# Kernel optimization log

Measured on AMD Instinct MI355X. Metric: run time of the kernel, lower is better.

## Reference

```python
import jax, jax.numpy as jnp
import numpy as np

B, T, D, E = 4096, 64, 256, 4
H = D * E  # hidden width per token position


def setup_inputs() -> dict:
    key = jax.random.key(0)
    kx, k1, kb1, k2, kb2 = jax.random.split(key, 5)
    # torch.nn.Linear default init ~ U(-1/sqrt(fan_in), 1/sqrt(fan_in)); scaled normals are fine for a numeric reference
    x = jax.random.normal(kx, (B, T, D), dtype=jnp.float32)
    W1 = jax.random.normal(k1, (T, D, H), dtype=jnp.float32) / np.sqrt(D)
    b1 = jax.random.normal(kb1, (T, H), dtype=jnp.float32) / np.sqrt(D)
    W2 = jax.random.normal(k2, (T, H, D), dtype=jnp.float32) / np.sqrt(H)
    b2 = jax.random.normal(kb2, (T, D), dtype=jnp.float32) / np.sqrt(H)
    return {"x": x, "W1": W1, "b1": b1, "W2": W2, "b2": b2}


def reference(x, W1, b1, W2, b2):
    # Per-position MLP with distinct weights: grouped GEMM over the T axis.
    h = jnp.einsum('btd,tdh->bth', x, W1) + b1          # [B, T, H]
    h = jax.nn.gelu(h, approximate=False)                # torch GELU default = exact erf form
    out = jnp.einsum('bth,thd->btd', h, W2) + b2         # [B, T, D]
    return out
```

## Files before the change

### kernel.cpp

```cpp
#include <hip/hip_runtime.h>


typedef __bf16 bf16x8 __attribute__((ext_vector_type(8)));
typedef float  floatx4 __attribute__((ext_vector_type(4)));

__device__ __forceinline__ unsigned short f2bf(float f) {
  unsigned u = __builtin_bit_cast(unsigned, f);
  u += 0x7fffu + ((u >> 16) & 1u);
  return (unsigned short)(u >> 16);
}

__device__ __forceinline__ float gelu_exact(float v) {
  return 0.5f * v * (1.0f + erff(v * 0.70710678118654752f));
}

__device__ __forceinline__ void gll16(const void* g, void* l) {
  __builtin_amdgcn_global_load_lds(
      (const __attribute__((address_space(1))) unsigned*)g,
      (__attribute__((address_space(3))) unsigned*)(unsigned)(unsigned long long)l,
      16, 0, 0);
}

__device__ __forceinline__ void barrier_fenced() {
  asm volatile("" ::: "memory");
  __builtin_amdgcn_s_barrier();
  asm volatile("" ::: "memory");
}


__global__ __launch_bounds__(256) void prep_w1(const float* __restrict__ w1,
                                               unsigned short* __restrict__ img) {
  const int idx  = blockIdx.x * 256 + threadIdx.x;
  const int slot = idx & 511;
  const int im   = idx >> 9;
  const int jl = slot >> 2, m = slot & 3;
  const int kk = im & 7, c = (im >> 3) & 7, t = im >> 6;
  const int q  = m ^ ((jl >> 1) & 3);
  const float* src = w1 + (size_t)t * 262144 +
                     (size_t)(kk * 32 + q * 8) * 1024 + c * 128 + jl;
  union { uint4 v; unsigned short s[8]; } o;
#pragma unroll
  for (int i = 0; i < 8; ++i) o.s[i] = f2bf(src[(size_t)i * 1024]);
  *(uint4*)(img + (size_t)idx * 8) = o.v;
}

__global__ __launch_bounds__(256) void prep_w2(const float* __restrict__ w2,
                                               unsigned short* __restrict__ img) {
  const int idx  = blockIdx.x * 256 + threadIdx.x;
  const int slot = idx & 1023;
  const int im   = idx >> 10;
  const int d = slot >> 2, m = slot & 3;
  const int kk2 = im & 3, c = (im >> 2) & 7, t = im >> 5;
  const int q   = m ^ ((d >> 1) & 3);
  const float* src = w2 + (size_t)t * 262144 +
                     (size_t)(c * 128 + kk2 * 32 + q * 8) * 256 + d;
  union { uint4 v; unsigned short s[8]; } o;
#pragma unroll
  for (int i = 0; i < 8; ++i) o.s[i] = f2bf(src[(size_t)i * 256]);
  *(uint4*)(img + (size_t)idx * 8) = o.v;
}

__global__ __launch_bounds__(256)
__attribute__((amdgpu_waves_per_eu(2, 2)))
void mlp_fast(
    const float* __restrict__ x, const unsigned short* __restrict__ w1i,
    const float* __restrict__ b1, const unsigned short* __restrict__ w2i,
    const float* __restrict__ b2, float* __restrict__ out) {

  __shared__ __attribute__((aligned(16))) unsigned char lds[69632];
  unsigned char* const w1b0 = lds;
  unsigned char* const w1b1 = lds + 8192;
  unsigned char* const w2b0 = lds + 16384;
  unsigned char* const w2b1 = lds + 32768;
  unsigned char* const hlds = lds + 49152;
  float* const b1lds = (float*)(lds + 65536);

  const int tid  = threadIdx.x;
  const int lane = tid & 63;
  const int w    = tid >> 6;
  const int wm   = w >> 1;
  const int wn   = w & 1;
  const int l15  = lane & 15;
  const int l4   = lane >> 4;

  const int bid  = blockIdx.x;
  const int t    = (bid & 7) + 8 * (bid >> 9);
  const int b0   = ((bid >> 3) & 63) << 6;

  const unsigned char* w1t = (const unsigned char*)(w1i + (size_t)t * 262144);
  const unsigned char* w2t = (const unsigned char*)(w2i + (size_t)t * 262144);
  const int lo16 = lane * 16;

#pragma unroll
  for (int i = 0; i < 4; ++i)
    b1lds[tid + 256 * i] = b1[t * 1024 + tid + 256 * i];

  bf16x8 xfrag[2][8];
#pragma unroll
  for (int mt = 0; mt < 2; ++mt) {
    const int b = b0 + wm * 32 + mt * 16 + l15;
    const float* xb = x + ((size_t)b * 64 + t) * 256 + l4 * 8;
#pragma unroll
    for (int kk = 0; kk < 8; ++kk) {
      floatx4 lo = *(const floatx4*)(xb + kk * 32);
      floatx4 hi = *(const floatx4*)(xb + kk * 32 + 4);
      union { bf16x8 v; unsigned short s[8]; } px;
      px.s[0] = f2bf(lo[0]); px.s[1] = f2bf(lo[1]);
      px.s[2] = f2bf(lo[2]); px.s[3] = f2bf(lo[3]);
      px.s[4] = f2bf(hi[0]); px.s[5] = f2bf(hi[1]);
      px.s[6] = f2bf(hi[2]); px.s[7] = f2bf(hi[3]);
      xfrag[mt][kk] = px.v;
    }
  }

  floatx4 oacc[4][4];
#pragma unroll
  for (int mt = 0; mt < 4; ++mt) {
    const floatx4 bv = *(const floatx4*)(b2 + t * 256 + w * 64 + mt * 16 + l4 * 4);
#pragma unroll
    for (int nt = 0; nt < 4; ++nt) oacc[mt][nt] = bv;
  }

  const int swf    = (l4 ^ ((lane >> 1) & 3)) << 4;
  const int w1base = ((wn * 64 + l15) << 6) + swf;
  const int w2base = ((w * 64 + l15) << 6) + swf;

  auto stageW1 = [&](int cc, int kk, unsigned char* buf) {
    const unsigned char* s = w1t + (((cc << 3) + kk) << 13) + (w << 11) + lo16;
    unsigned char* d = buf + (w << 11);
    gll16(s, d);
    gll16(s + 1024, d + 1024);
  };
  auto stageW2 = [&](int cc, int k2, unsigned char* buf) {
    const unsigned char* s = w2t + (((cc << 2) + k2) << 14) + (w << 12) + lo16;
    unsigned char* d = buf + (w << 12);
    gll16(s, d);               gll16(s + 1024, d + 1024);
    gll16(s + 2048, d + 2048); gll16(s + 3072, d + 3072);
  };

  stageW1(0, 0, w1b0);
  __syncthreads();

#pragma unroll 1
  for (int c = 0; c < 8; ++c) {
    floatx4 hacc[2][4];
#pragma unroll
    for (int nt = 0; nt < 4; ++nt) {
      const float bv = b1lds[c * 128 + wn * 64 + nt * 16 + l15];
      const floatx4 bb = {bv, bv, bv, bv};
      hacc[0][nt] = bb; hacc[1][nt] = bb;
    }

#pragma unroll
    for (int k = 0; k < 8; ++k) {
      if (k < 7) {
        stageW1(c, k + 1, ((k + 1) & 1) ? w1b1 : w1b0);
        asm volatile("s_waitcnt vmcnt(2)" ::: "memory");
      } else {
        stageW2(c, 0, w2b0);
        asm volatile("s_waitcnt vmcnt(4)" ::: "memory");
      }
      barrier_fenced();

      const unsigned char* rb = (k & 1) ? w1b1 : w1b0;
      bf16x8 bfrag[4];
#pragma unroll
      for (int nt = 0; nt < 4; ++nt)
        bfrag[nt] = *(const bf16x8*)(rb + w1base + nt * 1024);
      __builtin_amdgcn_s_setprio(1);
#pragma unroll
      for (int mt = 0; mt < 2; ++mt)
#pragma unroll
        for (int nt = 0; nt < 4; ++nt)
          hacc[mt][nt] = __builtin_amdgcn_mfma_f32_16x16x32_bf16(
              xfrag[mt][k], bfrag[nt], hacc[mt][nt], 0, 0, 0);
      __builtin_amdgcn_s_setprio(0);
      barrier_fenced();
    }

#pragma unroll
    for (int mt = 0; mt < 2; ++mt)
#pragma unroll
      for (int nt = 0; nt < 4; ++nt) {
        const int jl = wn * 64 + nt * 16 + l15;
        const int q  = jl >> 3;
        const int jo = (jl & 7) * 2;
#pragma unroll
        for (int r = 0; r < 4; ++r) {
          const float g = gelu_exact(hacc[mt][nt][r]);
          const int b = wm * 32 + mt * 16 + l4 * 4 + r;
          *(unsigned short*)(hlds + b * 256 + ((q ^ (b & 7)) * 16) + jo) = f2bf(g);
        }
      }

#pragma unroll
    for (int k2 = 0; k2 < 4; ++k2) {
      if (k2 < 3) {
        stageW2(c, k2 + 1, ((k2 + 1) & 1) ? w2b1 : w2b0);
        if (k2 == 0)
          asm volatile("s_waitcnt vmcnt(4) lgkmcnt(0)" ::: "memory");
        else
          asm volatile("s_waitcnt vmcnt(4)" ::: "memory");
      } else {
        if (c < 7) {
          stageW1(c + 1, 0, w1b0);
          asm volatile("s_waitcnt vmcnt(2)" ::: "memory");
        } else {
          asm volatile("s_waitcnt vmcnt(0)" ::: "memory");
        }
      }
      barrier_fenced();

      const unsigned char* rb = (k2 & 1) ? w2b1 : w2b0;
      bf16x8 afrag[4];
#pragma unroll
      for (int mt = 0; mt < 4; ++mt)
        afrag[mt] = *(const bf16x8*)(rb + w2base + mt * 1024);
      bf16x8 hfrag[4];
#pragma unroll
      for (int nt = 0; nt < 4; ++nt)
        hfrag[nt] = *(const bf16x8*)(hlds + (nt * 16 + l15) * 256 +
                                     (((k2 * 4 + l4) ^ (lane & 7)) * 16));
      __builtin_amdgcn_s_setprio(1);
#pragma unroll
      for (int mt = 0; mt < 4; ++mt)
#pragma unroll
        for (int nt = 0; nt < 4; ++nt)
          oacc[mt][nt] = __builtin_amdgcn_mfma_f32_16x16x32_bf16(
              afrag[mt], hfrag[nt], oacc[mt][nt], 0, 0, 0);
      __builtin_amdgcn_s_setprio(0);
      barrier_fenced();
    }
  }

#pragma unroll
  for (int mt = 0; mt < 4; ++mt) {
    const int d = w * 64 + mt * 16 + l4 * 4;
#pragma unroll
    for (int nt = 0; nt < 4; ++nt) {
      const int b = b0 + nt * 16 + l15;
      *(floatx4*)(out + ((size_t)b * 64 + t) * 256 + d) = oacc[mt][nt];
    }
  }
}

__global__ __launch_bounds__(256, 2) void mlp_kernel(
    const float* __restrict__ x, const float* __restrict__ w1,
    const float* __restrict__ b1, const float* __restrict__ w2,
    const float* __restrict__ b2, float* __restrict__ out) {

  __shared__ __attribute__((aligned(16))) unsigned char lds[40960];
  unsigned char* const w1img = lds;
  unsigned char* const w2img = lds + 8192;
  unsigned char* const hlds  = lds + 24576;

  const int tid  = threadIdx.x;
  const int lane = tid & 63;
  const int w    = tid >> 6;
  const int wm   = w >> 1;
  const int wn   = w & 1;
  const int l15  = lane & 15;
  const int l4   = lane >> 4;

  const int bid  = blockIdx.x;
  const int t    = (bid & 7) + 8 * (bid >> 9);
  const int b0   = ((bid >> 3) & 63) << 6;

  const float* w1t = w1 + (size_t)t * 262144;
  const float* w2t = w2 + (size_t)t * 262144;

  const int jl_s   = tid & 127;
  const int half_s = tid >> 7;
  const int P_s    = half_s ^ ((jl_s >> 2) & 1);
  const int sw2s   = (tid >> 1) & 3;

  bf16x8 xfrag[2][8];
#pragma unroll
  for (int mt = 0; mt < 2; ++mt) {
    const int b = b0 + wm * 32 + mt * 16 + l15;
    const float* xb = x + ((size_t)b * 64 + t) * 256 + l4 * 8;
#pragma unroll
    for (int kk = 0; kk < 8; ++kk) {
      floatx4 lo = *(const floatx4*)(xb + kk * 32);
      floatx4 hi = *(const floatx4*)(xb + kk * 32 + 4);
      union { bf16x8 v; unsigned short s[8]; } px;
      px.s[0] = f2bf(lo[0]); px.s[1] = f2bf(lo[1]);
      px.s[2] = f2bf(lo[2]); px.s[3] = f2bf(lo[3]);
      px.s[4] = f2bf(hi[0]); px.s[5] = f2bf(hi[1]);
      px.s[6] = f2bf(hi[2]); px.s[7] = f2bf(hi[3]);
      xfrag[mt][kk] = px.v;
    }
  }

  floatx4 oacc[4][4];
#pragma unroll
  for (int mt = 0; mt < 4; ++mt) {
    const floatx4 bv = *(const floatx4*)(b2 + t * 256 + w * 64 + mt * 16 + l4 * 4);
#pragma unroll
    for (int nt = 0; nt < 4; ++nt) oacc[mt][nt] = bv;
  }

  const int swf    = (l4 ^ ((lane >> 1) & 3)) << 4;
  const int w1base = ((wn * 64 + l15) << 6) + swf;
  const int w2base = ((w * 64 + l15) << 6) + swf;

#pragma unroll 1
  for (int c = 0; c < 8; ++c) {
    floatx4 hacc[2][4];
#pragma unroll
    for (int nt = 0; nt < 4; ++nt) {
      const float bv = b1[t * 1024 + c * 128 + wn * 64 + nt * 16 + l15];
      const floatx4 bb = {bv, bv, bv, bv};
      hacc[0][nt] = bb; hacc[1][nt] = bb;
    }

#pragma unroll
    for (int kk = 0; kk < 8; ++kk) {
      float f[16];
      const float* src = w1t + (size_t)(kk * 32 + half_s * 16) * 1024 + c * 128 + jl_s;
#pragma unroll
      for (int u = 0; u < 16; ++u) f[u] = src[(size_t)u * 1024];

      __syncthreads();
      union { uint4 v; unsigned short s[8]; } pk[2];
#pragma unroll
      for (int u = 0; u < 16; ++u) pk[u >> 3].s[u & 7] = f2bf(f[u]);
#pragma unroll
      for (int p = 0; p < 2; ++p) {
        const int m = 2 * P_s + p;
        const int s = (p ^ (jl_s >> 1)) & 1;
        *(uint4*)(w1img + jl_s * 64 + m * 16) = pk[s].v;
      }
      __syncthreads();

      bf16x8 bfrag[4];
#pragma unroll
      for (int nt = 0; nt < 4; ++nt)
        bfrag[nt] = *(const bf16x8*)(w1img + w1base + nt * 1024);
#pragma unroll
      for (int mt = 0; mt < 2; ++mt)
#pragma unroll
        for (int nt = 0; nt < 4; ++nt)
          hacc[mt][nt] = __builtin_amdgcn_mfma_f32_16x16x32_bf16(
              xfrag[mt][kk], bfrag[nt], hacc[mt][nt], 0, 0, 0);
    }

#pragma unroll
    for (int mt = 0; mt < 2; ++mt) {
#pragma unroll
      for (int nt = 0; nt < 4; ++nt) {
        const int jl = wn * 64 + nt * 16 + l15;
        const int q  = jl >> 3;
        const int jo = (jl & 7) * 2;
#pragma unroll
        for (int r = 0; r < 4; ++r) {
          const float g = gelu_exact(hacc[mt][nt][r]);
          const int b = wm * 32 + mt * 16 + l4 * 4 + r;
          *(unsigned short*)(hlds + b * 256 + ((q ^ (b & 7)) * 16) + jo) = f2bf(g);
        }
      }
    }

#pragma unroll
    for (int kk2 = 0; kk2 < 4; ++kk2) {
      float g2[32];
      const float* src2 = w2t + (size_t)(c * 128 + kk2 * 32) * 256 + tid;
#pragma unroll
      for (int v = 0; v < 32; ++v) g2[v] = src2[(size_t)v * 256];

      __syncthreads();
      union { uint4 v; unsigned short s[8]; } pk2[4];
#pragma unroll
      for (int v = 0; v < 32; ++v) pk2[v >> 3].s[v & 7] = f2bf(g2[v]);
#pragma unroll
      for (int p = 0; p < 4; ++p) {
        const int m = (p + (tid >> 1)) & 3;
        const int q = m ^ sw2s;
        *(uint4*)(w2img + tid * 64 + m * 16) = pk2[q].v;
      }
      __syncthreads();

      bf16x8 afrag[4];
#pragma unroll
      for (int mt = 0; mt < 4; ++mt)
        afrag[mt] = *(const bf16x8*)(w2img + w2base + mt * 1024);
      bf16x8 hfrag[4];
#pragma unroll
      for (int nt = 0; nt < 4; ++nt)
        hfrag[nt] = *(const bf16x8*)(hlds + (nt * 16 + l15) * 256 +
                                     (((kk2 * 4 + l4) ^ (lane & 7)) * 16));
#pragma unroll
      for (int mt = 0; mt < 4; ++mt)
#pragma unroll
        for (int nt = 0; nt < 4; ++nt)
          oacc[mt][nt] = __builtin_amdgcn_mfma_f32_16x16x32_bf16(
              afrag[mt], hfrag[nt], oacc[mt][nt], 0, 0, 0);
    }
  }

#pragma unroll
  for (int mt = 0; mt < 4; ++mt) {
    const int d = w * 64 + mt * 16 + l4 * 4;
#pragma unroll
    for (int nt = 0; nt < 4; ++nt) {
      const int b = b0 + nt * 16 + l15;
      *(floatx4*)(out + ((size_t)b * 64 + t) * 256 + d) = oacc[mt][nt];
    }
  }
}

extern "C" void kernel_launch(void* const* d_in, const int* in_sizes, int n_in,
                              void* d_out, int out_size, void* d_ws, size_t ws_size,
                              hipStream_t stream) {
  const float* x  = (const float*)d_in[0];
  const float* W1 = (const float*)d_in[1];
  const float* b1 = (const float*)d_in[2];
  const float* W2 = (const float*)d_in[3];
  const float* b2 = (const float*)d_in[4];
  float* out = (float*)d_out;

  const size_t need = 67108864;
  if (d_ws != nullptr && ws_size >= need) {
    unsigned short* w1img = (unsigned short*)d_ws;
    unsigned short* w2img = (unsigned short*)((char*)d_ws + 33554432);
    prep_w1<<<8192, 256, 0, stream>>>(W1, w1img);
    prep_w2<<<8192, 256, 0, stream>>>(W2, w2img);
    mlp_fast<<<4096, 256, 0, stream>>>(x, w1img, b1, w2img, b2, out);
  } else {
    mlp_kernel<<<4096, 256, 0, stream>>>(x, W1, b1, W2, b2, out);
  }
}
```

Before: 1.017 ms.

## Stream weight fragments directly to registers and coalesce weight prep via LDS

The prep kernels now read fp32 weights with coalesced vector loads, transpose and swizzle them through shared memory, and write the bf16 images in contiguous chunks, in place of scattered strided reads. The main kernel drops LDS staging of weights (global_load_lds double buffers and per-step barriers). Each wave instead loads its MFMA B/A fragments straight from global memory into registers, prefetching one step ahead. x is staged once into LDS as bf16 rather than held in registers, which frees registers for occupancy 3. The cost is that every wave does redundant global/L2 weight fetches with no cross-wave sharing.

New measurement: 1.029 ms. About the same (+1.2%).

```diff
diff --git a/kernel.cpp b/kernel.cpp
--- a/kernel.cpp
+++ b/kernel.cpp
@@ -14,66 +14,244 @@
   return 0.5f * v * (1.0f + erff(v * 0.70710678118654752f));
 }
 
-__device__ __forceinline__ void gll16(const void* g, void* l) {
-  __builtin_amdgcn_global_load_lds(
-      (const __attribute__((address_space(1))) unsigned*)g,
-      (__attribute__((address_space(3))) unsigned*)(unsigned)(unsigned long long)l,
-      16, 0, 0);
-}
-
-__device__ __forceinline__ void barrier_fenced() {
-  asm volatile("" ::: "memory");
-  __builtin_amdgcn_s_barrier();
-  asm volatile("" ::: "memory");
-}
-
 
 __global__ __launch_bounds__(256) void prep_w1(const float* __restrict__ w1,
                                                unsigned short* __restrict__ img) {
-  const int idx  = blockIdx.x * 256 + threadIdx.x;
-  const int slot = idx & 511;
-  const int im   = idx >> 9;
-  const int jl = slot >> 2, m = slot & 3;
-  const int kk = im & 7, c = (im >> 3) & 7, t = im >> 6;
-  const int q  = m ^ ((jl >> 1) & 3);
-  const float* src = w1 + (size_t)t * 262144 +
-                     (size_t)(kk * 32 + q * 8) * 1024 + c * 128 + jl;
-  union { uint4 v; unsigned short s[8]; } o;
-#pragma unroll
-  for (int i = 0; i < 8; ++i) o.s[i] = f2bf(src[(size_t)i * 1024]);
-  *(uint4*)(img + (size_t)idx * 8) = o.v;
+  __shared__ unsigned short simg[4096];
+  const int u = threadIdx.x, bid = blockIdx.x;
+  const int t = bid >> 3, kk = bid & 7;
+  const float* base = w1 + (size_t)t * 262144 + (size_t)(kk * 32) * 1024;
+  unsigned short* obase = img + (size_t)t * 262144 + kk * 4096;
+
+  for (int c = 0; c < 8; ++c) {
+#pragma unroll
+    for (int s = 0; s < 4; ++s) {
+      const int i = (s * 256 + u) * 4;
+      const int dl = i >> 7, col = i & 127;
+      floatx4 f = *(const floatx4*)(base + (size_t)dl * 1024 + c * 128 + col);
+      const int q = dl >> 3, i8 = dl & 7;
+#pragma unroll
+      for (int e = 0; e < 4; ++e) {
+        const int jl = col + e;
+        simg[jl * 32 + ((q ^ ((jl >> 1) & 3)) << 3) + i8] = f2bf(f[e]);
+      }
+    }
+    __syncthreads();
+    *(uint4*)(obase + (size_t)c * 32768 + u * 8) = *(const uint4*)(simg + u * 8);
+    *(uint4*)(obase + (size_t)c * 32768 + 2048 + u * 8) =
+        *(const uint4*)(simg + 2048 + u * 8);
+    __syncthreads();
+  }
 }
 
 __global__ __launch_bounds__(256) void prep_w2(const float* __restrict__ w2,
                                                unsigned short* __restrict__ img) {
-  const int idx  = blockIdx.x * 256 + threadIdx.x;
-  const int slot = idx & 1023;
-  const int im   = idx >> 10;
-  const int d = slot >> 2, m = slot & 3;
-  const int kk2 = im & 3, c = (im >> 2) & 7, t = im >> 5;
-  const int q   = m ^ ((d >> 1) & 3);
-  const float* src = w2 + (size_t)t * 262144 +
-                     (size_t)(c * 128 + kk2 * 32 + q * 8) * 256 + d;
-  union { uint4 v; unsigned short s[8]; } o;
-#pragma unroll
-  for (int i = 0; i < 8; ++i) o.s[i] = f2bf(src[(size_t)i * 256]);
-  *(uint4*)(img + (size_t)idx * 8) = o.v;
-}
-
-__global__ __launch_bounds__(256)
-__attribute__((amdgpu_waves_per_eu(2, 2)))
-void mlp_fast(
+  __shared__ unsigned short simg[8192];
+  const int u = threadIdx.x, bid = blockIdx.x;
+  const int t = bid >> 3, c = bid & 7;
+  const float* base = w2 + (size_t)t * 262144 + (size_t)(c * 128) * 256;
+  unsigned short* obase = img + (size_t)t * 262144 + c * 32768;
+
+  for (int kk2 = 0; kk2 < 4; ++kk2) {
+#pragma unroll
+    for (int s = 0; s < 8; ++s) {
+      const int i = (s * 256 + u) * 4;
+      const int jr = i >> 8, d = i & 255;
+      floatx4 f = *(const floatx4*)(base + (size_t)(kk2 * 32 + jr) * 256 + d);
+      const int q = jr >> 3, i8 = jr & 7;
+#pragma unroll
+      for (int e = 0; e < 4; ++e) {
+        const int dd = d + e;
+        simg[dd * 32 + ((q ^ ((dd >> 1) & 3)) << 3) + i8] = f2bf(f[e]);
+      }
+    }
+    __syncthreads();
+#pragma unroll
+    for (int r = 0; r < 4; ++r)
+      *(uint4*)(obase + (size_t)kk2 * 8192 + (r * 256 + u) * 8) =
+          *(const uint4*)(simg + (r * 256 + u) * 8);
+    __syncthreads();
+  }
+}
+
+__global__ __launch_bounds__(256, 3) void mlp_fast2(
     const float* __restrict__ x, const unsigned short* __restrict__ w1i,
     const float* __restrict__ b1, const unsigned short* __restrict__ w2i,
     const float* __restrict__ b2, float* __restrict__ out) {
 
-  __shared__ __attribute__((aligned(16))) unsigned char lds[69632];
-  unsigned char* const w1b0 = lds;
-  unsigned char* const w1b1 = lds + 8192;
-  unsigned char* const w2b0 = lds + 16384;
-  unsigned char* const w2b1 = lds + 32768;
-  unsigned char* const hlds = lds + 49152;
-  float* const b1lds = (float*)(lds + 65536);
+  __shared__ __attribute__((aligned(16))) unsigned char lds[53248];
+  unsigned char* const xlds = lds;
+  unsigned char* const hlds = lds + 32768;
+  float* const b1lds = (float*)(lds + 49152);
+
+  const int tid  = threadIdx.x;
+  const int lane = tid & 63;
+  const int w    = tid >> 6, wm = w >> 1, wn = w & 1;
+  const int l15  = lane & 15, l4 = lane >> 4;
+
+  const int bid = blockIdx.x;
+  const int t   = (bid & 7) + 8 * (bid >> 9);
+  const int b0  = ((bid >> 3) & 63) << 6;
+
+  const unsigned char* w1t = (const unsigned char*)(w1i + (size_t)t * 262144);
+  const unsigned char* w2t = (const unsigned char*)(w2i + (size_t)t * 262144);
+
+#pragma unroll
+  for (int i = 0; i < 4; ++i)
+    b1lds[tid + 256 * i] = b1[t * 1024 + tid + 256 * i];
+
+  {
+    const int bl = tid >> 2, seg = tid & 3;
+    const float* xr = x + ((size_t)(b0 + bl) * 64 + t) * 256 + seg * 64;
+#pragma unroll
+    for (int g = 0; g < 8; ++g) {
+      const int d = seg * 64 + g * 8;
+      floatx4 lo = *(const floatx4*)(xr + g * 8);
+      floatx4 hi = *(const floatx4*)(xr + g * 8 + 4);
+      union { uint4 v; unsigned short s[8]; } px;
+      px.s[0] = f2bf(lo[0]); px.s[1] = f2bf(lo[1]);
+      px.s[2] = f2bf(lo[2]); px.s[3] = f2bf(lo[3]);
+      px.s[4] = f2bf(hi[0]); px.s[5] = f2bf(hi[1]);
+      px.s[6] = f2bf(hi[2]); px.s[7] = f2bf(hi[3]);
+      const int k = d >> 5, slot = (d >> 3) & 3;
+      *(uint4*)(xlds + k * 4096 + bl * 64 + ((slot ^ (bl & 3)) << 4)) = px.v;
+    }
+  }
+
+  floatx4 oacc[4][4];
+#pragma unroll
+  for (int mt = 0; mt < 4; ++mt) {
+    const floatx4 bv = *(const floatx4*)(b2 + t * 256 + w * 64 + mt * 16 + l4 * 4);
+#pragma unroll
+    for (int nt = 0; nt < 4; ++nt) oacc[mt][nt] = bv;
+  }
+
+  __syncthreads();
+
+  const int swf    = (l4 ^ ((lane >> 1) & 3)) << 4;
+  const int w1base = ((wn * 64 + l15) << 6) + swf;
+  const int w2base = ((w * 64 + l15) << 6) + swf;
+  const int xbase  = (wm * 32 + l15) * 64 + ((l4 ^ (l15 & 3)) << 4);
+
+  bf16x8 bcur[4];
+#pragma unroll
+  for (int nt = 0; nt < 4; ++nt)
+    bcur[nt] = *(const bf16x8*)(w1t + w1base + nt * 1024);
+
+#pragma unroll 1
+  for (int c = 0; c < 8; ++c) {
+    floatx4 hacc[2][4];
+#pragma unroll
+    for (int nt = 0; nt < 4; ++nt) {
+      const float bv = b1lds[c * 128 + wn * 64 + nt * 16 + l15];
+      const floatx4 bb = {bv, bv, bv, bv};
+      hacc[0][nt] = bb; hacc[1][nt] = bb;
+    }
+
+#pragma unroll
+    for (int k = 0; k < 8; ++k) {
+      const int s = c * 8 + k;
+      const unsigned char* nsrc =
+          w1t + (size_t)((s < 63 ? s + 1 : 63) * 8192);
+      bf16x8 bnxt[4];
+#pragma unroll
+      for (int nt = 0; nt < 4; ++nt)
+        bnxt[nt] = *(const bf16x8*)(nsrc + w1base + nt * 1024);
+      const bf16x8 xf0 = *(const bf16x8*)(xlds + k * 4096 + xbase);
+      const bf16x8 xf1 = *(const bf16x8*)(xlds + k * 4096 + xbase + 1024);
+      __builtin_amdgcn_s_setprio(1);
+#pragma unroll
+      for (int nt = 0; nt < 4; ++nt) {
+        hacc[0][nt] = __builtin_amdgcn_mfma_f32_16x16x32_bf16(
+            xf0, bcur[nt], hacc[0][nt], 0, 0, 0);
+        hacc[1][nt] = __builtin_amdgcn_mfma_f32_16x16x32_bf16(
+            xf1, bcur[nt], hacc[1][nt], 0, 0, 0);
+      }
+      __builtin_amdgcn_s_setprio(0);
+#pragma unroll
+      for (int nt = 0; nt < 4; ++nt) bcur[nt] = bnxt[nt];
+    }
+
+#pragma unroll
+    for (int mt = 0; mt < 2; ++mt)
+#pragma unroll
+      for (int nt = 0; nt < 4; ++nt) {
+        const int jl = wn * 64 + nt * 16 + l15;
+        const int q  = jl >> 3;
+        const int jo = (jl & 7) * 2;
+#pragma unroll
+        for (int r = 0; r < 4; ++r) {
+          const float g = gelu_exact(hacc[mt][nt][r]);
+          const int b = wm * 32 + mt * 16 + l4 * 4 + r;
+          *(unsigned short*)(hlds + b * 256 + ((q ^ (b & 7)) * 16) + jo) = f2bf(g);
+        }
+      }
+
+    bf16x8 acur[4];
+    {
+      const unsigned char* asrc = w2t + (size_t)(c * 4) * 16384;
+#pragma unroll
+      for (int mt = 0; mt < 4; ++mt)
+        acur[mt] = *(const bf16x8*)(asrc + w2base + mt * 1024);
+    }
+
+    asm volatile("s_waitcnt lgkmcnt(0)" ::: "memory");
+    __builtin_amdgcn_s_barrier();
+    asm volatile("" ::: "memory");
+
+#pragma unroll
+    for (int k2 = 0; k2 < 4; ++k2) {
+      bf16x8 anxt[4];
+      if (k2 < 3) {
+        const unsigned char* nsrc2 = w2t + (size_t)(c * 4 + k2 + 1) * 16384;
+#pragma unroll
+        for (int mt = 0; mt < 4; ++mt)
+          anxt[mt] = *(const bf16x8*)(nsrc2 + w2base + mt * 1024);
+      }
+      bf16x8 hfr[4];
+#pragma unroll
+      for (int nt = 0; nt < 4; ++nt)
+        hfr[nt] = *(const bf16x8*)(hlds + (nt * 16 + l15) * 256 +
+                                   (((k2 * 4 + l4) ^ (lane & 7)) * 16));
+      __builtin_amdgcn_s_setprio(1);
+#pragma unroll
+      for (int mt = 0; mt < 4; ++mt)
+#pragma unroll
+        for (int nt = 0; nt < 4; ++nt)
+          oacc[mt][nt] = __builtin_amdgcn_mfma_f32_16x16x32_bf16(
+              acur[mt], hfr[nt], oacc[mt][nt], 0, 0, 0);
+      __builtin_amdgcn_s_setprio(0);
+      if (k2 < 3) {
+#pragma unroll
+        for (int mt = 0; mt < 4; ++mt) acur[mt] = anxt[mt];
+      }
+    }
+
+    asm volatile("s_waitcnt lgkmcnt(0)" ::: "memory");
+    __builtin_amdgcn_s_barrier();
+    asm volatile("" ::: "memory");
+  }
+
+#pragma unroll
+  for (int mt = 0; mt < 4; ++mt) {
+    const int d = w * 64 + mt * 16 + l4 * 4;
+#pragma unroll
+    for (int nt = 0; nt < 4; ++nt) {
+      const int b = b0 + nt * 16 + l15;
+      *(floatx4*)(out + ((size_t)b * 64 + t) * 256 + d) = oacc[mt][nt];
+    }
+  }
+}
+
+__global__ __launch_bounds__(256, 2) void mlp_kernel(
+    const float* __restrict__ x, const float* __restrict__ w1,
+    const float* __restrict__ b1, const float* __restrict__ w2,
+    const float* __restrict__ b2, float* __restrict__ out) {
+
+  __shared__ __attribute__((aligned(16))) unsigned char lds[40960];
+  unsigned char* const w1img = lds;
+  unsigned char* const w2img = lds + 8192;
+  unsigned char* const hlds  = lds + 24576;
 
   const int tid  = threadIdx.x;
   const int lane = tid & 63;
@@ -87,13 +265,13 @@
   const int t    = (bid & 7) + 8 * (bid >> 9);
   const int b0   = ((bid >> 3) & 63) << 6;
 
-  const unsigned char* w1t = (const unsigned char*)(w1i + (size_t)t * 262144);
-  const unsigned char* w2t = (const unsigned char*)(w2i + (size_t)t * 262144);
-  const int lo16 = lane * 16;
-
-#pragma unroll
-  for (int i = 0; i < 4; ++i)
-    b1lds[tid + 256 * i] = b1[t * 1024 + tid + 256 * i];
+  const float* w1t = w1 + (size_t)t * 262144;
+  const float* w2t = w2 + (size_t)t * 262144;
+
+  const int jl_s   = tid & 127;
+  const int half_s = tid >> 7;
+  const int P_s    = half_s ^ ((jl_s >> 2) & 1);
+  const int sw2s   = (tid >> 1) & 3;
 
   bf16x8 xfrag[2][8];
 #pragma unroll
@@ -125,185 +303,6 @@
   const int w1base = ((wn * 64 + l15) << 6) + swf;
   const int w2base = ((w * 64 + l15) << 6) + swf;
 
-  auto stageW1 = [&](int cc, int kk, unsigned char* buf) {
-    const unsigned char* s = w1t + (((cc << 3) + kk) << 13) + (w << 11) + lo16;
-    unsigned char* d = buf + (w << 11);
-    gll16(s, d);
-    gll16(s + 1024, d + 1024);
-  };
-  auto stageW2 = [&](int cc, int k2, unsigned char* buf) {
-    const unsigned char* s = w2t + (((cc << 2) + k2) << 14) + (w << 12) + lo16;
-    unsigned char* d = buf + (w << 12);
-    gll16(s, d);               gll16(s + 1024, d + 1024);
-    gll16(s + 2048, d + 2048); gll16(s + 3072, d + 3072);
-  };
-
-  stageW1(0, 0, w1b0);
-  __syncthreads();
-
-#pragma unroll 1
-  for (int c = 0; c < 8; ++c) {
-    floatx4 hacc[2][4];
-#pragma unroll
-    for (int nt = 0; nt < 4; ++nt) {
-      const float bv = b1lds[c * 128 + wn * 64 + nt * 16 + l15];
-      const floatx4 bb = {bv, bv, bv, bv};
-      hacc[0][nt] = bb; hacc[1][nt] = bb;
-    }
-
-#pragma unroll
-    for (int k = 0; k < 8; ++k) {
-      if (k < 7) {
-        stageW1(c, k + 1, ((k + 1) & 1) ? w1b1 : w1b0);
-        asm volatile("s_waitcnt vmcnt(2)" ::: "memory");
-      } else {
-        stageW2(c, 0, w2b0);
-        asm volatile("s_waitcnt vmcnt(4)" ::: "memory");
-      }
-      barrier_fenced();
-
-      const unsigned char* rb = (k & 1) ? w1b1 : w1b0;
-      bf16x8 bfrag[4];
-#pragma unroll
-      for (int nt = 0; nt < 4; ++nt)
-        bfrag[nt] = *(const bf16x8*)(rb + w1base + nt * 1024);
-      __builtin_amdgcn_s_setprio(1);
-#pragma unroll
-      for (int mt = 0; mt < 2; ++mt)
-#pragma unroll
-        for (int nt = 0; nt < 4; ++nt)
-          hacc[mt][nt] = __builtin_amdgcn_mfma_f32_16x16x32_bf16(
-              xfrag[mt][k], bfrag[nt], hacc[mt][nt], 0, 0, 0);
-      __builtin_amdgcn_s_setprio(0);
-      barrier_fenced();
-    }
-
-#pragma unroll
-    for (int mt = 0; mt < 2; ++mt)
-#pragma unroll
-      for (int nt = 0; nt < 4; ++nt) {
-        const int jl = wn * 64 + nt * 16 + l15;
-        const int q  = jl >> 3;
-        const int jo = (jl & 7) * 2;
-#pragma unroll
-        for (int r = 0; r < 4; ++r) {
-          const float g = gelu_exact(hacc[mt][nt][r]);
-          const int b = wm * 32 + mt * 16 + l4 * 4 + r;
-          *(unsigned short*)(hlds + b * 256 + ((q ^ (b & 7)) * 16) + jo) = f2bf(g);
-        }
-      }
-
-#pragma unroll
-    for (int k2 = 0; k2 < 4; ++k2) {
-      if (k2 < 3) {
-        stageW2(c, k2 + 1, ((k2 + 1) & 1) ? w2b1 : w2b0);
-        if (k2 == 0)
-          asm volatile("s_waitcnt vmcnt(4) lgkmcnt(0)" ::: "memory");
-        else
-          asm volatile("s_waitcnt vmcnt(4)" ::: "memory");
-      } else {
-        if (c < 7) {
-          stageW1(c + 1, 0, w1b0);
-          asm volatile("s_waitcnt vmcnt(2)" ::: "memory");
-        } else {
-          asm volatile("s_waitcnt vmcnt(0)" ::: "memory");
-        }
-      }
-      barrier_fenced();
-
-      const unsigned char* rb = (k2 & 1) ? w2b1 : w2b0;
-      bf16x8 afrag[4];
-#pragma unroll
-      for (int mt = 0; mt < 4; ++mt)
-        afrag[mt] = *(const bf16x8*)(rb + w2base + mt * 1024);
-      bf16x8 hfrag[4];
-#pragma unroll
-      for (int nt = 0; nt < 4; ++nt)
-        hfrag[nt] = *(const bf16x8*)(hlds + (nt * 16 + l15) * 256 +
-                                     (((k2 * 4 + l4) ^ (lane & 7)) * 16));
-      __builtin_amdgcn_s_setprio(1);
-#pragma unroll
-      for (int mt = 0; mt < 4; ++mt)
-#pragma unroll
-        for (int nt = 0; nt < 4; ++nt)
-          oacc[mt][nt] = __builtin_amdgcn_mfma_f32_16x16x32_bf16(
-              afrag[mt], hfrag[nt], oacc[mt][nt], 0, 0, 0);
-      __builtin_amdgcn_s_setprio(0);
-      barrier_fenced();
-    }
-  }
-
-#pragma unroll
-  for (int mt = 0; mt < 4; ++mt) {
-    const int d = w * 64 + mt * 16 + l4 * 4;
-#pragma unroll
-    for (int nt = 0; nt < 4; ++nt) {
-      const int b = b0 + nt * 16 + l15;
-      *(floatx4*)(out + ((size_t)b * 64 + t) * 256 + d) = oacc[mt][nt];
-    }
-  }
-}
-
-__global__ __launch_bounds__(256, 2) void mlp_kernel(
-    const float* __restrict__ x, const float* __restrict__ w1,
-    const float* __restrict__ b1, const float* __restrict__ w2,
-    const float* __restrict__ b2, float* __restrict__ out) {
-
-  __shared__ __attribute__((aligned(16))) unsigned char lds[40960];
-  unsigned char* const w1img = lds;
-  unsigned char* const w2img = lds + 8192;
-  unsigned char* const hlds  = lds + 24576;
-
-  const int tid  = threadIdx.x;
-  const int lane = tid & 63;
-  const int w    = tid >> 6;
-  const int wm   = w >> 1;
-  const int wn   = w & 1;
-  const int l15  = lane & 15;
-  const int l4   = lane >> 4;
-
-  const int bid  = blockIdx.x;
-  const int t    = (bid & 7) + 8 * (bid >> 9);
-  const int b0   = ((bid >> 3) & 63) << 6;
-
-  const float* w1t = w1 + (size_t)t * 262144;
-  const float* w2t = w2 + (size_t)t * 262144;
-
-  const int jl_s   = tid & 127;
-  const int half_s = tid >> 7;
-  const int P_s    = half_s ^ ((jl_s >> 2) & 1);
-  const int sw2s   = (tid >> 1) & 3;
-
-  bf16x8 xfrag[2][8];
-#pragma unroll
-  for (int mt = 0; mt < 2; ++mt) {
-    const int b = b0 + wm * 32 + mt * 16 + l15;
-    const float* xb = x + ((size_t)b * 64 + t) * 256 + l4 * 8;
-#pragma unroll
-    for (int kk = 0; kk < 8; ++kk) {
-      floatx4 lo = *(const floatx4*)(xb + kk * 32);
-      floatx4 hi = *(const floatx4*)(xb + kk * 32 + 4);
-      union { bf16x8 v; unsigned short s[8]; } px;
-      px.s[0] = f2bf(lo[0]); px.s[1] = f2bf(lo[1]);
-      px.s[2] = f2bf(lo[2]); px.s[3] = f2bf(lo[3]);
-      px.s[4] = f2bf(hi[0]); px.s[5] = f2bf(hi[1]);
-      px.s[6] = f2bf(hi[2]); px.s[7] = f2bf(hi[3]);
-      xfrag[mt][kk] = px.v;
-    }
-  }
-
-  floatx4 oacc[4][4];
-#pragma unroll
-  for (int mt = 0; mt < 4; ++mt) {
-    const floatx4 bv = *(const floatx4*)(b2 + t * 256 + w * 64 + mt * 16 + l4 * 4);
-#pragma unroll
-    for (int nt = 0; nt < 4; ++nt) oacc[mt][nt] = bv;
-  }
-
-  const int swf    = (l4 ^ ((lane >> 1) & 3)) << 4;
-  const int w1base = ((wn * 64 + l15) << 6) + swf;
-  const int w2base = ((w * 64 + l15) << 6) + swf;
-
 #pragma unroll 1
   for (int c = 0; c < 8; ++c) {
     floatx4 hacc[2][4];
@@ -423,9 +422,9 @@
   if (d_ws != nullptr && ws_size >= need) {
     unsigned short* w1img = (unsigned short*)d_ws;
     unsigned short* w2img = (unsigned short*)((char*)d_ws + 33554432);
-    prep_w1<<<8192, 256, 0, stream>>>(W1, w1img);
-    prep_w2<<<8192, 256, 0, stream>>>(W2, w2img);
-    mlp_fast<<<4096, 256, 0, stream>>>(x, w1img, b1, w2img, b2, out);
+    prep_w1<<<512, 256, 0, stream>>>(W1, w1img);
+    prep_w2<<<512, 256, 0, stream>>>(W2, w2img);
+    mlp_fast2<<<4096, 256, 0, stream>>>(x, w1img, b1, w2img, b2, out);
   } else {
     mlp_kernel<<<4096, 256, 0, stream>>>(x, W1, b1, W2, b2, out);
   }
```
